# Kernel optimization log

Hardware: AMD Instinct MI355X
Metric: run time of the kernel (lower is better)

The kernel has to match this reference:

```python
import jax, jax.numpy as jnp
import numpy as np

B, N, Hg, Wg, C = 2, 6, 28, 60, 128
NUM_POINTS, EXTENT = 4, 0.5
IMG_W, IMG_H = 480.0, 224.0
PC_RANGE = np.array([-50.0, -50.0, -4.0, 50.0, 50.0, 4.0], dtype=np.float32)


def setup_inputs() -> dict:
    key = jax.random.key(0)
    ks = jax.random.split(key, 8)
    lo = jnp.asarray(PC_RANGE[:3])
    hi = jnp.asarray(PC_RANGE[3:])
    means3D = jax.random.uniform(ks[0], (B * N, Hg, Wg, 3)) * (hi - lo) + lo
    dv = jax.random.normal(ks[1], (B * N, Hg, Wg, 3))
    dv = dv / (jnp.linalg.norm(dv, axis=-1, keepdims=True) + 1e-6)
    A = jax.random.normal(ks[2], (B * N, Hg, Wg, 3, 3)) * 0.3
    cov3D = jnp.einsum('...ik,...jk->...ij', A, A) + 1e-4 * jnp.eye(3)
    img_features = jax.random.normal(ks[3], (B * N, C, Hg, Wg))
    lidar2img = jax.random.normal(ks[4], (B, N, 4, 4))
    W1 = jax.random.normal(ks[5], (3, 2 * C)) * 0.1
    b1 = jnp.zeros((2 * C,))
    W2 = jax.random.normal(ks[6], (2 * C, C)) * 0.1
    b2 = jnp.zeros((C,))
    return {'means3D': means3D, 'img_features': img_features,
            'direction_vector': dv, 'cov3D': cov3D, 'lidar2img': lidar2img,
            'W1': W1, 'b1': b1, 'W2': W2, 'b2': b2}


def grid_sample_bilinear(feat, grid):
    """feat: (B,C,H,W); grid: (B,L,P,2) in [-1,1]; align_corners=False, zeros padding.
    Returns (B,L,P,C)."""
    Bn, Cc, H, W = feat.shape
    x = (grid[..., 0] + 1.0) * (W * 0.5) - 0.5
    y = (grid[..., 1] + 1.0) * (H * 0.5) - 0.5
    x0 = jnp.floor(x)
    y0 = jnp.floor(y)
    wx = x - x0
    wy = y - y0
    bi = jnp.arange(Bn).reshape(Bn, 1, 1)

    def gather(yi, xi):
        valid = (xi >= 0) & (xi < W) & (yi >= 0) & (yi < H)
        xc = jnp.clip(xi, 0, W - 1).astype(jnp.int32)
        yc = jnp.clip(yi, 0, H - 1).astype(jnp.int32)
        g = feat[bi, :, yc, xc]  # (B,L,P,C)
        return g * valid[..., None].astype(feat.dtype)

    v00 = gather(y0, x0)
    v01 = gather(y0, x0 + 1)
    v10 = gather(y0 + 1, x0)
    v11 = gather(y0 + 1, x0 + 1)
    wx = wx[..., None]
    wy = wy[..., None]
    return (v00 * (1 - wx) * (1 - wy) + v01 * wx * (1 - wy)
            + v10 * (1 - wx) * wy + v11 * wx * wy)


def _forward(means3D, img_features, direction_vector, cov3D, lidar2img, W1, b1, W2, b2):
    b, n = lidar2img.shape[:2]
    L = Hg * Wg
    means = means3D.reshape(b, n, L, 3)
    dv = direction_vector.reshape(b, n, L, 3)
    cov = cov3D.reshape(b, n, L, 3, 3)

    # uncertainty along direction vector: 5 steps in [-1.5, 1.5]
    lin5 = jnp.linspace(-1.5, 1.5, 5)
    q = jnp.einsum('bnli,bnlij,bnlj->bnl', dv, cov, dv)
    unc = lin5 * jnp.sqrt(q)[..., None, None] * dv[..., :, None]  # b n l 3 5
    means_unc = means[..., None] + unc                            # b n l 3 5

    # orthogonal vector: cross(dv, (0,0,1)) = (dv_y, -dv_x, 0)
    orth = jnp.stack([dv[..., 1], -dv[..., 0], jnp.zeros_like(dv[..., 0])], axis=-1)
    linP = jnp.linspace(-EXTENT, EXTENT, NUM_POINTS)
    offs = orth[..., None] * linP                                 # b n l 3 p
    pts = offs[..., None, :] + means_unc[..., None]               # b n l 3 5 p
    pts = pts.transpose(0, 1, 2, 4, 5, 3).reshape(b, n, L, 5 * NUM_POINTS, 3)

    # project to cameras
    ones = jnp.ones(pts.shape[:-1] + (1,), pts.dtype)
    pts_h = jnp.concatenate([pts, ones], axis=-1)
    cam = jnp.einsum('bnij,bnlpj->bnlpi', lidar2img, pts_h)
    homo = jnp.maximum(cam[..., 2:3], 1e-6)
    cam_xy = cam[..., 0:2] / homo
    cam_out = cam_xy
    grid = jnp.stack([cam_xy[..., 0] / IMG_W, cam_xy[..., 1] / IMG_H], axis=-1) * 2.0 - 1.0
    grid = grid.reshape(b * n, L, 5 * NUM_POINTS, 2)
    feats = grid_sample_bilinear(img_features, grid)
    feats = feats.reshape(b, n, L, 5 * NUM_POINTS, -1)

    # positional encoding on pc_range-normalized points
    lo = jnp.asarray(PC_RANGE[:3])
    hi = jnp.asarray(PC_RANGE[3:])
    pn = jnp.clip((pts - lo) / (hi - lo), 0.0, 1.0)
    pe = jax.nn.relu(pn @ W1 + b1) @ W2 + b2
    feats = feats + pe

    P2 = 5 * NUM_POINTS
    return (feats.reshape(b, n * L, P2, -1), cam_out, pts.reshape(b, n * L, P2, 3))


def reference(means3D, img_features, direction_vector, cov3D, lidar2img, W1, b1, W2, b2):
    return _forward(means3D, img_features, direction_vector, cov3D, lidar2img, W1, b1, W2, b2)
```

## Files before the change

### kernel.cpp

```cpp
#include <hip/hip_runtime.h>
#include <math.h>

#define BN 12
#define HG 28
#define WG 60
#define LL 1680
#define CC 128
#define P2 20
#define HID 256
#define NPTS (BN * LL * P2)
#define NPB 64
#define NWG (NPTS / NPB)
#define NQB 4
#define NP (NQB * P2)

static constexpr size_t OUT_CAM_OFF = (size_t)BN * LL * P2 * CC;
static constexpr size_t OUT_PTS_OFF = OUT_CAM_OFF + (size_t)BN * LL * P2 * 2;

typedef short v8s __attribute__((ext_vector_type(8)));
typedef float v4f __attribute__((ext_vector_type(4)));
typedef unsigned long long u64;

__device__ __forceinline__ unsigned short f2bf(float f) {
  unsigned x = __float_as_uint(f);
  unsigned r = (x + 0x7FFFu + ((x >> 16) & 1u)) >> 16;
  return (unsigned short)r;
}

__global__ __launch_bounds__(256) void transpose_feat_k(const float* __restrict__ in,
                                                        float* __restrict__ out) {
  __shared__ float tile[64][65];
  const int bn = blockIdx.z;
  const int c0 = blockIdx.y * 64;
  const int l0 = blockIdx.x * 64;
  const int t = threadIdx.x;
  {
    const int lx = t & 63;
    const int cy = t >> 6;
#pragma unroll
    for (int i = 0; i < 64; i += 4) {
      const int c = c0 + cy + i;
      const int l = l0 + lx;
      float v = 0.f;
      if (l < LL) v = in[((size_t)bn * CC + c) * LL + l];
      tile[cy + i][lx] = v;
    }
  }
  __syncthreads();
  {
    const int cx = t & 63;
    const int ly = t >> 6;
#pragma unroll
    for (int i = 0; i < 64; i += 4) {
      const int l = l0 + ly + i;
      const int c = c0 + cx;
      if (l < LL) out[((size_t)bn * LL + l) * CC + c] = tile[cx][ly + i];
    }
  }
}

__global__ __launch_bounds__(256) void pack_w2_k(const float* __restrict__ W2,
                                                 unsigned short* __restrict__ W2bf) {
  const int t = blockIdx.x * 256 + threadIdx.x;
  if (t >= 4096) return;
  const int lane = t & 63;
  const int ks = (t >> 6) & 7;
  const int cg = t >> 9;
  const int col = cg * 16 + (lane & 15);
  const int kb = ks * 32 + (lane >> 4) * 8;
  v8s r;
#pragma unroll
  for (int e = 0; e < 8; ++e) r[e] = (short)f2bf(W2[(size_t)(kb + e) * CC + col]);
  *(v8s*)(W2bf + (size_t)t * 8) = r;
}

__global__ __launch_bounds__(256) void geom_k(const float* __restrict__ means3D,
                                              const float* __restrict__ dvec,
                                              const float* __restrict__ cov3D,
                                              const float* __restrict__ l2i,
                                              float* __restrict__ out,
                                              u64* __restrict__ off8,
                                              float4* __restrict__ w4,
                                              float4* __restrict__ pn4) {
  const int pid = blockIdx.x * 256 + threadIdx.x;
  if (pid >= NPTS) return;
  const unsigned qg = (unsigned)pid / P2;
  const int p = pid - (int)qg * P2;
  const unsigned bn = qg / LL;

  const size_t base3 = (size_t)qg * 3;
  const float m0 = means3D[base3 + 0], m1 = means3D[base3 + 1], m2 = means3D[base3 + 2];
  const float d0 = dvec[base3 + 0], d1 = dvec[base3 + 1], d2 = dvec[base3 + 2];
  const float* cv = cov3D + (size_t)qg * 9;
  const float q = d0 * (cv[0] * d0 + cv[1] * d1 + cv[2] * d2) +
                  d1 * (cv[3] * d0 + cv[4] * d1 + cv[5] * d2) +
                  d2 * (cv[6] * d0 + cv[7] * d1 + cv[8] * d2);
  const float s = sqrtf(q);
  const int k = p >> 2, j = p & 3;
  const float a = (-1.5f + 0.75f * (float)k) * s;
  const float tt = -0.5f + (1.0f / 3.0f) * (float)j;
  const float px = m0 + a * d0 + tt * d1;
  const float py = m1 + a * d1 - tt * d0;
  const float pz = m2 + a * d2;
  const float* M = l2i + (size_t)bn * 16;
  const float cx = M[0] * px + M[1] * py + M[2] * pz + M[3];
  const float cy = M[4] * px + M[5] * py + M[6] * pz + M[7];
  const float cz = M[8] * px + M[9] * py + M[10] * pz + M[11];
  const float homo = fmaxf(cz, 1e-6f);
  const float u = cx / homo;
  const float v = cy / homo;

  *(float2*)(out + OUT_CAM_OFF + (size_t)pid * 2) = make_float2(u, v);
  float* ptso = out + OUT_PTS_OFF + (size_t)pid * 3;
  ptso[0] = px;
  ptso[1] = py;
  ptso[2] = pz;

  const float x = u * 0.125f - 0.5f;
  const float y = v * 0.125f - 0.5f;
  const float x0f = floorf(x), y0f = floorf(y);
  const float wx = x - x0f, wy = y - y0f;
  const bool vx0 = (x0f >= 0.f) && (x0f < (float)WG);
  const bool vx1 = (x0f + 1.f >= 0.f) && (x0f + 1.f < (float)WG);
  const bool vy0 = (y0f >= 0.f) && (y0f < (float)HG);
  const bool vy1 = (y0f + 1.f >= 0.f) && (y0f + 1.f < (float)HG);
  const unsigned ix0 = (unsigned)(int)fminf(fmaxf(x0f, 0.f), (float)(WG - 1));
  const unsigned ix1 = (unsigned)(int)fminf(fmaxf(x0f + 1.f, 0.f), (float)(WG - 1));
  const unsigned iy0 = (unsigned)(int)fminf(fmaxf(y0f, 0.f), (float)(HG - 1));
  const unsigned iy1 = (unsigned)(int)fminf(fmaxf(y0f + 1.f, 0.f), (float)(HG - 1));
  const u64 o0 = (u64)(iy0 * WG + ix0);
  const u64 o1 = (u64)(iy0 * WG + ix1);
  const u64 o2 = (u64)(iy1 * WG + ix0);
  const u64 o3 = (u64)(iy1 * WG + ix1);
  off8[pid] = o0 | (o1 << 16) | (o2 << 32) | (o3 << 48);
  w4[pid] = make_float4((vx0 && vy0) ? (1.f - wx) * (1.f - wy) : 0.f,
                        (vx1 && vy0) ? wx * (1.f - wy) : 0.f,
                        (vx0 && vy1) ? (1.f - wx) * wy : 0.f,
                        (vx1 && vy1) ? wx * wy : 0.f);
  pn4[pid] = make_float4(fminf(fmaxf((px + 50.f) * 0.01f, 0.f), 1.f),
                         fminf(fmaxf((py + 50.f) * 0.01f, 0.f), 1.f),
                         fminf(fmaxf((pz + 4.f) * 0.125f, 0.f), 1.f), 0.f);
}

__global__ __launch_bounds__(256, 4) void gemm_k(
    const float* __restrict__ featT,
    const float* __restrict__ W1,
    const float* __restrict__ b1,
    const unsigned short* __restrict__ W2bf,
    const float* __restrict__ b2,
    const u64* __restrict__ off8,
    const float4* __restrict__ w4,
    const float4* __restrict__ pn4,
    float* __restrict__ out) {
  const int tid = threadIdx.x;

  const int orig = blockIdx.x;
  const int xcd = orig & 7;
  const int pos = orig >> 3;
  const int wgid = (xcd < 4 ? xcd * 788 : 4 * 788 + (xcd - 4) * 787) + pos;
  if (wgid >= NWG) return;

  const int gp0 = wgid * NPB;
  const int bn = wgid / 525;

  __shared__ __align__(16) char sH[NPB * 512];
  __shared__ u64 sOff8[NPB];
  __shared__ float4 sWl[NPB];
  __shared__ float4 sPnl[NPB];

  if (tid < NPB) {
    sOff8[tid] = off8[gp0 + tid];
    sWl[tid] = w4[gp0 + tid];
    sPnl[tid] = pn4[gp0 + tid];
  }

  const int wv = tid >> 6;
  const int lane = tid & 63;
  const int lrow = lane & 15;
  const int g = lane >> 4;

  v8s fb0[8], fb1[8];
#pragma unroll
  for (int ks = 0; ks < 8; ++ks) {
    fb0[ks] = *(const v8s*)(W2bf + (size_t)(((wv * 2 + 0) * 8 + ks) * 64 + lane) * 8);
    fb1[ks] = *(const v8s*)(W2bf + (size_t)(((wv * 2 + 1) * 8 + ks) * 64 + lane) * 8);
  }

  const int h4 = (tid & 63) * 4;
  const int pw = tid >> 6;
  const float4 a0 = *(const float4*)(W1 + h4);
  const float4 a1 = *(const float4*)(W1 + HID + h4);
  const float4 a2 = *(const float4*)(W1 + 2 * HID + h4);
  const float4 bb = *(const float4*)(b1 + h4);

  __syncthreads();

#pragma unroll
  for (int it = 0; it < NPB / 4; ++it) {
    const int p = it * 4 + pw;
    const float4 pn = sPnl[p];
    const float v0 = fmaxf(bb.x + pn.x * a0.x + pn.y * a1.x + pn.z * a2.x, 0.f);
    const float v1 = fmaxf(bb.y + pn.x * a0.y + pn.y * a1.y + pn.z * a2.y, 0.f);
    const float v2 = fmaxf(bb.z + pn.x * a0.z + pn.y * a1.z + pn.z * a2.z, 0.f);
    const float v3 = fmaxf(bb.w + pn.x * a0.w + pn.y * a1.w + pn.z * a2.w, 0.f);
    const u64 pk = (u64)f2bf(v0) | ((u64)f2bf(v1) << 16) | ((u64)f2bf(v2) << 32) |
                   ((u64)f2bf(v3) << 48);
    *(u64*)(sH + p * 512 + (((unsigned)(h4 * 2)) ^ (((unsigned)(p & 7)) << 4))) = pk;
  }
  __syncthreads();

  for (int pt = 0; pt < 4; ++pt) {
    const int arow = pt * 16 + lrow;
    const unsigned swz = ((unsigned)(arow & 7)) << 4;
    v8s fa[8];
#pragma unroll
    for (int ks = 0; ks < 8; ++ks)
      fa[ks] = *(const v8s*)(sH + arow * 512 + (((unsigned)(ks * 64 + g * 16)) ^ swz));
    v4f acc0 = {0.f, 0.f, 0.f, 0.f};
    v4f acc1 = {0.f, 0.f, 0.f, 0.f};
#pragma unroll
    for (int ks = 0; ks < 8; ++ks)
      acc0 = __builtin_amdgcn_mfma_f32_16x16x32_bf16(fa[ks], fb0[ks], acc0, 0, 0, 0);
#pragma unroll
    for (int ks = 0; ks < 8; ++ks)
      acc1 = __builtin_amdgcn_mfma_f32_16x16x32_bf16(fa[ks], fb1[ks], acc1, 0, 0, 0);
    __syncthreads();
#pragma unroll
    for (int r = 0; r < 4; ++r) {
      const int lp = pt * 16 + g * 4 + r;
      const unsigned s2 = ((unsigned)(lp & 7)) << 4;
      const int c0 = wv * 32 + lrow;
      *(float*)(sH + lp * 512 + (((unsigned)(c0 * 4)) ^ s2)) = acc0[r];
      *(float*)(sH + lp * 512 + (((unsigned)((c0 + 16) * 4)) ^ s2)) = acc1[r];
    }
    __syncthreads();
  }

  const float* featc = featT + (size_t)bn * (LL * CC);
#pragma unroll
  for (int it = 0; it < 8; ++it) {
    const int p = it * 8 + (tid >> 5);
    const int c4g = tid & 31;
    const unsigned boff =
        (unsigned)(p * 512) + (((unsigned)(c4g * 16)) ^ (((unsigned)(p & 7)) << 4));
    const v4f t = *(const v4f*)(sH + boff);
    const u64 o8 = sOff8[p];
    const float4 w = sWl[p];
    const float4 bias = *(const float4*)(b2 + c4g * 4);
    float rx = t[0] + bias.x, ry = t[1] + bias.y, rz = t[2] + bias.z, rw = t[3] + bias.w;
    {
      const float4 f = *(const float4*)(featc + (size_t)(unsigned)(o8 & 0xFFFFu) * CC + c4g * 4);
      rx += w.x * f.x; ry += w.x * f.y; rz += w.x * f.z; rw += w.x * f.w;
    }
    {
      const float4 f =
          *(const float4*)(featc + (size_t)(unsigned)((o8 >> 16) & 0xFFFFu) * CC + c4g * 4);
      rx += w.y * f.x; ry += w.y * f.y; rz += w.y * f.z; rw += w.y * f.w;
    }
    {
      const float4 f =
          *(const float4*)(featc + (size_t)(unsigned)((o8 >> 32) & 0xFFFFu) * CC + c4g * 4);
      rx += w.z * f.x; ry += w.z * f.y; rz += w.z * f.z; rw += w.z * f.w;
    }
    {
      const float4 f =
          *(const float4*)(featc + (size_t)(unsigned)((o8 >> 48) & 0xFFFFu) * CC + c4g * 4);
      rx += w.w * f.x; ry += w.w * f.y; rz += w.w * f.z; rw += w.w * f.w;
    }
    *(float4*)(out + (size_t)(gp0 + p) * CC + c4g * 4) = make_float4(rx, ry, rz, rw);
  }
}

__global__ __launch_bounds__(128) void gauss_fb(
    const float* __restrict__ means3D, const float* __restrict__ feat,
    const float* __restrict__ dvec, const float* __restrict__ cov3D,
    const float* __restrict__ l2i, const float* __restrict__ W1,
    const float* __restrict__ b1, const float* __restrict__ W2,
    const float* __restrict__ b2, float* __restrict__ out) {
  const int l = blockIdx.x;
  const int bn = blockIdx.y;
  const int tid = threadIdx.x;
  __shared__ float sH[P2][HID];
  __shared__ float sPn[P2][3];
  __shared__ float sW[P2][4];
  __shared__ int sOff[P2][4];
  if (tid < P2) {
    const int p = tid;
    const size_t base3 = ((size_t)bn * LL + l) * 3;
    const float m0 = means3D[base3 + 0], m1 = means3D[base3 + 1], m2 = means3D[base3 + 2];
    const float d0 = dvec[base3 + 0], d1 = dvec[base3 + 1], d2 = dvec[base3 + 2];
    const float* cv = cov3D + ((size_t)bn * LL + l) * 9;
    const float q = d0 * (cv[0] * d0 + cv[1] * d1 + cv[2] * d2) +
                    d1 * (cv[3] * d0 + cv[4] * d1 + cv[5] * d2) +
                    d2 * (cv[6] * d0 + cv[7] * d1 + cv[8] * d2);
    const float s = sqrtf(q);
    const int k = p >> 2, j = p & 3;
    const float a = (-1.5f + 0.75f * (float)k) * s;
    const float tt = -0.5f + (1.0f / 3.0f) * (float)j;
    const float px = m0 + a * d0 + tt * d1;
    const float py = m1 + a * d1 - tt * d0;
    const float pz = m2 + a * d2;
    const float* M = l2i + (size_t)bn * 16;
    const float cx = M[0] * px + M[1] * py + M[2] * pz + M[3];
    const float cy = M[4] * px + M[5] * py + M[6] * pz + M[7];
    const float cz = M[8] * px + M[9] * py + M[10] * pz + M[11];
    const float homo = fmaxf(cz, 1e-6f);
    const float u = cx / homo;
    const float v = cy / homo;
    float* camo = out + OUT_CAM_OFF + (((size_t)bn * LL + l) * P2 + p) * 2;
    camo[0] = u;
    camo[1] = v;
    float* ptso = out + OUT_PTS_OFF + (((size_t)bn * LL + l) * P2 + p) * 3;
    ptso[0] = px;
    ptso[1] = py;
    ptso[2] = pz;
    const float x = u * 0.125f - 0.5f;
    const float y = v * 0.125f - 0.5f;
    const float x0f = floorf(x), y0f = floorf(y);
    const float wx = x - x0f, wy = y - y0f;
    const bool vx0 = (x0f >= 0.f) && (x0f < (float)WG);
    const bool vx1 = (x0f + 1.f >= 0.f) && (x0f + 1.f < (float)WG);
    const bool vy0 = (y0f >= 0.f) && (y0f < (float)HG);
    const bool vy1 = (y0f + 1.f >= 0.f) && (y0f + 1.f < (float)HG);
    const int ix0 = (int)fminf(fmaxf(x0f, 0.f), (float)(WG - 1));
    const int ix1 = (int)fminf(fmaxf(x0f + 1.f, 0.f), (float)(WG - 1));
    const int iy0 = (int)fminf(fmaxf(y0f, 0.f), (float)(HG - 1));
    const int iy1 = (int)fminf(fmaxf(y0f + 1.f, 0.f), (float)(HG - 1));
    sOff[p][0] = iy0 * WG + ix0;
    sOff[p][1] = iy0 * WG + ix1;
    sOff[p][2] = iy1 * WG + ix0;
    sOff[p][3] = iy1 * WG + ix1;
    sW[p][0] = (vx0 && vy0) ? (1.f - wx) * (1.f - wy) : 0.f;
    sW[p][1] = (vx1 && vy0) ? wx * (1.f - wy) : 0.f;
    sW[p][2] = (vx0 && vy1) ? (1.f - wx) * wy : 0.f;
    sW[p][3] = (vx1 && vy1) ? wx * wy : 0.f;
    sPn[p][0] = fminf(fmaxf((px + 50.f) * 0.01f, 0.f), 1.f);
    sPn[p][1] = fminf(fmaxf((py + 50.f) * 0.01f, 0.f), 1.f);
    sPn[p][2] = fminf(fmaxf((pz + 4.f) * 0.125f, 0.f), 1.f);
  }
  __syncthreads();
  for (int u0 = tid; u0 < P2 * HID; u0 += 128) {
    const int p = u0 >> 8;
    const int h = u0 & (HID - 1);
    const float v = b1[h] + sPn[p][0] * W1[h] + sPn[p][1] * W1[HID + h] + sPn[p][2] * W1[2 * HID + h];
    sH[p][h] = fmaxf(v, 0.f);
  }
  __syncthreads();
  const int pg = tid >> 5;
  const int c0 = (tid & 31) * 4;
  const int pbase = pg * 5;
  float acc[5][4];
#pragma unroll
  for (int i = 0; i < 5; ++i)
#pragma unroll
    for (int j2 = 0; j2 < 4; ++j2) acc[i][j2] = 0.f;
  for (int h = 0; h < HID; h += 4) {
    const float4 w0 = *(const float4*)(W2 + (size_t)(h + 0) * CC + c0);
    const float4 w1 = *(const float4*)(W2 + (size_t)(h + 1) * CC + c0);
    const float4 w2 = *(const float4*)(W2 + (size_t)(h + 2) * CC + c0);
    const float4 w3 = *(const float4*)(W2 + (size_t)(h + 3) * CC + c0);
#pragma unroll
    for (int i = 0; i < 5; ++i) {
      const float4 hv = *(const float4*)(&sH[pbase + i][h]);
      acc[i][0] += hv.x * w0.x + hv.y * w1.x + hv.z * w2.x + hv.w * w3.x;
      acc[i][1] += hv.x * w0.y + hv.y * w1.y + hv.z * w2.y + hv.w * w3.y;
      acc[i][2] += hv.x * w0.z + hv.y * w1.z + hv.z * w2.z + hv.w * w3.z;
      acc[i][3] += hv.x * w0.w + hv.y * w1.w + hv.z * w2.w + hv.w * w3.w;
    }
  }
  const float4 bias = *(const float4*)(b2 + c0);
  const float* fbase = feat + (size_t)bn * CC * LL;
#pragma unroll
  for (int i = 0; i < 5; ++i) {
    const int p = pbase + i;
    float4 r;
    r.x = acc[i][0] + bias.x;
    r.y = acc[i][1] + bias.y;
    r.z = acc[i][2] + bias.z;
    r.w = acc[i][3] + bias.w;
#pragma unroll
    for (int corner = 0; corner < 4; ++corner) {
      const float w = sW[p][corner];
      const int off = sOff[p][corner];
      r.x += w * fbase[(size_t)(c0 + 0) * LL + off];
      r.y += w * fbase[(size_t)(c0 + 1) * LL + off];
      r.z += w * fbase[(size_t)(c0 + 2) * LL + off];
      r.w += w * fbase[(size_t)(c0 + 3) * LL + off];
    }
    *(float4*)(out + (((size_t)bn * LL + l) * P2 + p) * CC + c0) = r;
  }
}

extern "C" void kernel_launch(void* const* d_in, const int* in_sizes, int n_in,
                              void* d_out, int out_size, void* d_ws, size_t ws_size,
                              hipStream_t stream) {
  const float* means3D = (const float*)d_in[0];
  const float* img = (const float*)d_in[1];
  const float* dvec = (const float*)d_in[2];
  const float* cov3D = (const float*)d_in[3];
  const float* l2i = (const float*)d_in[4];
  const float* W1 = (const float*)d_in[5];
  const float* b1 = (const float*)d_in[6];
  const float* W2 = (const float*)d_in[7];
  const float* b2 = (const float*)d_in[8];
  float* out = (float*)d_out;

  const size_t w2bf_bytes = 65536;
  const size_t tbytes = (size_t)BN * LL * CC * sizeof(float);
  const size_t off8_bytes = (size_t)NPTS * 8;
  const size_t w4_bytes = (size_t)NPTS * 16;
  const size_t need_full = w2bf_bytes + tbytes + off8_bytes + 2 * w4_bytes;

  if (ws_size >= need_full) {
    unsigned short* W2bf = (unsigned short*)d_ws;
    float* featT = (float*)((char*)d_ws + w2bf_bytes);
    u64* off8 = (u64*)((char*)d_ws + w2bf_bytes + tbytes);
    float4* w4 = (float4*)((char*)d_ws + w2bf_bytes + tbytes + off8_bytes);
    float4* pn4 = (float4*)((char*)d_ws + w2bf_bytes + tbytes + off8_bytes + w4_bytes);
    hipLaunchKernelGGL(pack_w2_k, dim3(16), dim3(256), 0, stream, W2, W2bf);
    hipLaunchKernelGGL(transpose_feat_k, dim3((LL + 63) / 64, CC / 64, BN), dim3(256), 0,
                       stream, img, featT);
    hipLaunchKernelGGL(geom_k, dim3(NPTS / 256), dim3(256), 0, stream, means3D, dvec, cov3D,
                       l2i, out, off8, w4, pn4);
    hipLaunchKernelGGL(gemm_k, dim3(NWG), dim3(256), 0, stream, featT, W1, b1, W2bf, b2,
                       off8, w4, pn4, out);
  } else {
    hipLaunchKernelGGL(gauss_fb, dim3(LL, BN), dim3(128), 0, stream, means3D, img, dvec, cov3D,
                       l2i, W1, b1, W2, b2, out);
  }
}
```

Baseline: 99.98 us.

## Batch MFMA tiles in pairs, drop XCD remap, use packed bf16 conversion

The GEMM loop now computes two 16-row point tiles before each pair of barriers, halving the number of __syncthreads between MFMA compute and the in-place write-back to shared memory. Manual bf16 rounding is replaced by the packed __float22bfloat162_rn intrinsic. The XCD-aware workgroup remapping is removed in favor of plain blockIdx ordering. Holding more accumulators raises register pressure, and dropping the remap may change L2 locality of feature gathers.

```diff
diff --git a/kernel.cpp b/kernel.cpp
--- a/kernel.cpp
+++ b/kernel.cpp
@@ -1,4 +1,5 @@
 #include <hip/hip_runtime.h>
+#include <hip/hip_bf16.h>
 #include <math.h>
 
 #define BN 12
@@ -11,8 +12,6 @@
 #define NPTS (BN * LL * P2)
 #define NPB 64
 #define NWG (NPTS / NPB)
-#define NQB 4
-#define NP (NQB * P2)
 
 static constexpr size_t OUT_CAM_OFF = (size_t)BN * LL * P2 * CC;
 static constexpr size_t OUT_PTS_OFF = OUT_CAM_OFF + (size_t)BN * LL * P2 * 2;
@@ -153,13 +152,7 @@
     const float4* __restrict__ pn4,
     float* __restrict__ out) {
   const int tid = threadIdx.x;
-
-  const int orig = blockIdx.x;
-  const int xcd = orig & 7;
-  const int pos = orig >> 3;
-  const int wgid = (xcd < 4 ? xcd * 788 : 4 * 788 + (xcd - 4) * 787) + pos;
-  if (wgid >= NWG) return;
-
+  const int wgid = blockIdx.x;
   const int gp0 = wgid * NPB;
   const int bn = wgid / 525;
 
@@ -203,35 +196,51 @@
     const float v1 = fmaxf(bb.y + pn.x * a0.y + pn.y * a1.y + pn.z * a2.y, 0.f);
     const float v2 = fmaxf(bb.z + pn.x * a0.z + pn.y * a1.z + pn.z * a2.z, 0.f);
     const float v3 = fmaxf(bb.w + pn.x * a0.w + pn.y * a1.w + pn.z * a2.w, 0.f);
-    const u64 pk = (u64)f2bf(v0) | ((u64)f2bf(v1) << 16) | ((u64)f2bf(v2) << 32) |
-                   ((u64)f2bf(v3) << 48);
+    __hip_bfloat162 plo = __float22bfloat162_rn(make_float2(v0, v1));
+    __hip_bfloat162 phi = __float22bfloat162_rn(make_float2(v2, v3));
+    const unsigned ulo = *reinterpret_cast<const unsigned*>(&plo);
+    const unsigned uhi = *reinterpret_cast<const unsigned*>(&phi);
+    const u64 pk = (u64)ulo | ((u64)uhi << 32);
     *(u64*)(sH + p * 512 + (((unsigned)(h4 * 2)) ^ (((unsigned)(p & 7)) << 4))) = pk;
   }
   __syncthreads();
 
-  for (int pt = 0; pt < 4; ++pt) {
-    const int arow = pt * 16 + lrow;
-    const unsigned swz = ((unsigned)(arow & 7)) << 4;
-    v8s fa[8];
-#pragma unroll
-    for (int ks = 0; ks < 8; ++ks)
-      fa[ks] = *(const v8s*)(sH + arow * 512 + (((unsigned)(ks * 64 + g * 16)) ^ swz));
-    v4f acc0 = {0.f, 0.f, 0.f, 0.f};
-    v4f acc1 = {0.f, 0.f, 0.f, 0.f};
-#pragma unroll
-    for (int ks = 0; ks < 8; ++ks)
-      acc0 = __builtin_amdgcn_mfma_f32_16x16x32_bf16(fa[ks], fb0[ks], acc0, 0, 0, 0);
-#pragma unroll
-    for (int ks = 0; ks < 8; ++ks)
-      acc1 = __builtin_amdgcn_mfma_f32_16x16x32_bf16(fa[ks], fb1[ks], acc1, 0, 0, 0);
+#pragma unroll
+  for (int pg2 = 0; pg2 < 2; ++pg2) {
+    v4f acc[2][2];
+#pragma unroll
+    for (int i = 0; i < 2; ++i)
+#pragma unroll
+      for (int c = 0; c < 2; ++c) acc[i][c] = (v4f){0.f, 0.f, 0.f, 0.f};
+
+#pragma unroll
+    for (int pth = 0; pth < 2; ++pth) {
+      const int pt = pg2 * 2 + pth;
+      const int arow = pt * 16 + lrow;
+      const unsigned swz = ((unsigned)(arow & 7)) << 4;
+      v8s fa[8];
+#pragma unroll
+      for (int ks = 0; ks < 8; ++ks)
+        fa[ks] = *(const v8s*)(sH + arow * 512 + (((unsigned)(ks * 64 + g * 16)) ^ swz));
+#pragma unroll
+      for (int ks = 0; ks < 8; ++ks)
+        acc[pth][0] = __builtin_amdgcn_mfma_f32_16x16x32_bf16(fa[ks], fb0[ks], acc[pth][0], 0, 0, 0);
+#pragma unroll
+      for (int ks = 0; ks < 8; ++ks)
+        acc[pth][1] = __builtin_amdgcn_mfma_f32_16x16x32_bf16(fa[ks], fb1[ks], acc[pth][1], 0, 0, 0);
+    }
     __syncthreads();
 #pragma unroll
-    for (int r = 0; r < 4; ++r) {
-      const int lp = pt * 16 + g * 4 + r;
-      const unsigned s2 = ((unsigned)(lp & 7)) << 4;
-      const int c0 = wv * 32 + lrow;
-      *(float*)(sH + lp * 512 + (((unsigned)(c0 * 4)) ^ s2)) = acc0[r];
-      *(float*)(sH + lp * 512 + (((unsigned)((c0 + 16) * 4)) ^ s2)) = acc1[r];
+    for (int pth = 0; pth < 2; ++pth) {
+      const int pt = pg2 * 2 + pth;
+#pragma unroll
+      for (int r = 0; r < 4; ++r) {
+        const int lp = pt * 16 + g * 4 + r;
+        const unsigned s2 = ((unsigned)(lp & 7)) << 4;
+        const int c0 = wv * 32 + lrow;
+        *(float*)(sH + lp * 512 + (((unsigned)(c0 * 4)) ^ s2)) = acc[pth][0][r];
+        *(float*)(sH + lp * 512 + (((unsigned)((c0 + 16) * 4)) ^ s2)) = acc[pth][1][r];
+      }
     }
     __syncthreads();
   }
```

After: 98.06 us. No clear change (-1.9%).
